# Kernel optimization log

Measured on AMD Instinct MI355X. Metric: run time of the kernel, lower is better.

## Reference

```python
import jax, jax.numpy as jnp
import numpy as np

MARGIN = 1.0
B, C = 64, 206

def setup_inputs() -> dict:
    key = jax.random.key(0)
    k1, k2, k3 = jax.random.split(key, 3)
    preds = jax.random.normal(k1, (B, C), dtype=jnp.float32)
    sample_weights = jax.random.uniform(k2, (B,), dtype=jnp.float32)
    labels = jax.random.randint(k3, (B, C), 0, 2, dtype=jnp.int32)
    return {"preds": preds, "sample_weights": sample_weights, "labels": labels}

def reference(preds, sample_weights, labels):
    # Faithful AUCLoss: mean over pos x neg pairs of log(1+exp(-(p-n)*margin)) * w_pos * w_neg.
    # Data-dependent boolean gathers are replaced by multiplicative masks (identical math):
    # masked entries contribute 0, and we divide by n_pos*n_neg (the masked-matrix size).
    pos_mask = (labels == 1)
    neg_mask = (labels == 0)
    # per-element weight = per-sample weight broadcast over classes
    w = jnp.broadcast_to(sample_weights[:, None], labels.shape)
    p = preds.reshape(-1)                      # [N]
    pw = jnp.where(pos_mask.reshape(-1), w.reshape(-1), 0.0)  # [N] pos weights (0 where not pos)
    nw = jnp.where(neg_mask.reshape(-1), w.reshape(-1), 0.0)  # [N] neg weights (0 where not neg)
    diff = p[:, None] - p[None, :]             # [N, N] pairwise diffs (pos rows, neg cols)
    loss_matrix = jax.nn.softplus(-diff * MARGIN)  # == log(1 + exp(-diff*margin)), stable
    weighted_sum = jnp.einsum('ij,i,j->', loss_matrix, pw, nw)
    n_pos = pos_mask.sum().astype(preds.dtype)
    n_neg = neg_mask.sum().astype(preds.dtype)
    return weighted_sum / (n_pos * n_neg)
```

## Files before the change

kernel.cpp:

```cpp
#include <hip/hip_runtime.h>

#define NB 64
#define NC 206
#define N (NB * NC)
#define IPT 4
#define GX 13
#define NGPR 52
#define NBLK (GX * NB)
#define LN2F 0.69314718056f

struct Ws {
    double partials[NBLK];
};

__global__ __launch_bounds__(256) void pairs_kernel(
    const float* __restrict__ preds,
    const float* __restrict__ sw,
    const int* __restrict__ labels,
    double* __restrict__ partials)
{
    const int bx   = blockIdx.x;
    const int row  = blockIdx.y;
    const int lane = threadIdx.x & 63;
    const int wid  = threadIdx.x >> 6;

    __shared__ float sEGf[NGPR * 4];
    __shared__ float wsum[4];

    {
        const int c = threadIdx.x;
        if (c < NGPR * 4) {
            float e = 0.0f;
            if (c < NC) {
                float p = preds[row * NC + c];
                int   l = labels[row * NC + c];
                e = (l == 0) ? __expf(p) : 0.0f;
            }
            sEGf[c] = e;
        }
    }

    float F[IPT], PW[IPT], acc[IPT];
    #pragma unroll
    for (int k = 0; k < IPT; ++k) {
        int i = bx * 1024 + k * 256 + threadIdx.x;
        if (i < N) {
            float p = preds[i];
            int   l = labels[i];
            F[k]  = __expf(-p);
            PW[k] = (l == 1) ? sw[i / NC] : 0.0f;
        } else {
            F[k] = 0.0f; PW[k] = 0.0f;
        }
        acc[k] = 0.0f;
    }
    __syncthreads();

    const float4* sEG = (const float4*)sEGf;

    #pragma unroll 2
    for (int g = 0; g < NGPR; ++g) {
        float4 e = sEG[g];
        #pragma unroll
        for (int k = 0; k < IPT; ++k) {
            float t0 = fmaf(e.x, F[k], 1.0f);
            float t1 = fmaf(e.y, F[k], 1.0f);
            float t2 = fmaf(e.z, F[k], 1.0f);
            float t3 = fmaf(e.w, F[k], 1.0f);
            float m  = (t0 * t1) * (t2 * t3);
            acc[k] += __log2f(m);
        }
    }

    float a = 0.0f;
    #pragma unroll
    for (int k = 0; k < IPT; ++k) a = fmaf(acc[k], PW[k], a);
    a *= sw[row] * LN2F;

    #pragma unroll
    for (int off = 32; off > 0; off >>= 1)
        a += __shfl_down(a, off, 64);

    if (lane == 0) wsum[wid] = a;
    __syncthreads();
    if (threadIdx.x == 0)
        partials[row * GX + bx] = (double)(wsum[0] + wsum[1] + wsum[2] + wsum[3]);
}

__global__ __launch_bounds__(256) void reduce_kernel(
    const int* __restrict__ labels,
    const Ws* __restrict__ ws,
    float* __restrict__ out)
{
    const int lane = threadIdx.x & 63;
    const int wid  = threadIdx.x >> 6;

    double s = 0.0;
    for (int t = threadIdx.x; t < NBLK; t += 256)
        s += ws->partials[t];

    int pc = 0;
    const int4* l4 = (const int4*)labels;
    for (int t = threadIdx.x; t < N / 4; t += 256) {
        int4 v = l4[t];
        pc += v.x + v.y + v.z + v.w;
    }

    #pragma unroll
    for (int off = 32; off > 0; off >>= 1) {
        s  += __shfl_down(s, off, 64);
        pc += __shfl_down(pc, off, 64);
    }

    __shared__ double ds[4];
    __shared__ int    dp[4];
    if (lane == 0) { ds[wid] = s; dp[wid] = pc; }
    __syncthreads();
    if (threadIdx.x == 0) {
        double total = ds[0] + ds[1] + ds[2] + ds[3];
        int npos     = dp[0] + dp[1] + dp[2] + dp[3];
        double denom = (double)npos * (double)(N - npos);
        out[0] = (float)(total / denom);
    }
}

extern "C" void kernel_launch(void* const* d_in, const int* in_sizes, int n_in,
                              void* d_out, int out_size, void* d_ws, size_t ws_size,
                              hipStream_t stream)
{
    const float* preds  = (const float*)d_in[0];
    const float* sw     = (const float*)d_in[1];
    const int*   labels = (const int*)d_in[2];
    float* out = (float*)d_out;
    Ws* ws = (Ws*)d_ws;

    dim3 grid(GX, NB);
    pairs_kernel<<<grid, 256, 0, stream>>>(preds, sw, labels, ws->partials);

    reduce_kernel<<<1, 256, 0, stream>>>(labels, ws, out);
}
```

Measured before the change: 22.55 us.

## Compact positive elements into shared memory and batch eight negatives per log

Each block uses wave ballots and prefix counts to compact only the positive-labelled elements of its chunk into shared memory, then runs the pairwise loop only over those, skipping the roughly half of work spent on zero-weight rows. The product trick is widened from four to eight negatives per log2, halving transcendental calls. This adds extra shared memory, two barriers and a serial segment scan, and multiplying eight factors raises the risk of float overflow for large exp values.

```diff
diff --git a/kernel.cpp b/kernel.cpp
--- a/kernel.cpp
+++ b/kernel.cpp
@@ -3,9 +3,8 @@
 #define NB 64
 #define NC 206
 #define N (NB * NC)
-#define IPT 4
 #define GX 13
-#define NGPR 52
+#define NG8 26
 #define NBLK (GX * NB)
 #define LN2F 0.69314718056f
 
@@ -21,69 +20,106 @@
 {
     const int bx   = blockIdx.x;
     const int row  = blockIdx.y;
-    const int lane = threadIdx.x & 63;
-    const int wid  = threadIdx.x >> 6;
+    const int tid  = threadIdx.x;
+    const int lane = tid & 63;
+    const int wave = tid >> 6;
 
-    __shared__ float sEGf[NGPR * 4];
+    __shared__ float sEGf[NG8 * 8];
+    __shared__ float sF[1024], sPW[1024];
+    __shared__ int   segCnt[16];
     __shared__ float wsum[4];
 
-    {
-        const int c = threadIdx.x;
-        if (c < NGPR * 4) {
-            float e = 0.0f;
-            if (c < NC) {
-                float p = preds[row * NC + c];
-                int   l = labels[row * NC + c];
-                e = (l == 0) ? __expf(p) : 0.0f;
-            }
-            sEGf[c] = e;
+    if (tid < NG8 * 8) {
+        float e = 0.0f;
+        if (tid < NC) {
+            float p = preds[row * NC + tid];
+            int   l = labels[row * NC + tid];
+            e = (l == 0) ? __expf(p) : 0.0f;
         }
+        sEGf[tid] = e;
     }
 
-    float F[IPT], PW[IPT], acc[IPT];
+    float pv[4]; float wv[4]; unsigned int rank[4]; bool act[4];
+    unsigned long long pre = (1ull << lane) - 1ull;
     #pragma unroll
-    for (int k = 0; k < IPT; ++k) {
-        int i = bx * 1024 + k * 256 + threadIdx.x;
+    for (int k = 0; k < 4; ++k) {
+        int i = bx * 1024 + k * 256 + tid;
+        bool a = false; float p = 0.0f, w = 0.0f;
         if (i < N) {
-            float p = preds[i];
-            int   l = labels[i];
-            F[k]  = __expf(-p);
-            PW[k] = (l == 1) ? sw[i / NC] : 0.0f;
-        } else {
-            F[k] = 0.0f; PW[k] = 0.0f;
+            p = preds[i];
+            a = (labels[i] == 1);
+            if (a) w = sw[i / NC];
         }
-        acc[k] = 0.0f;
+        unsigned long long ball = __ballot(a);
+        if (lane == 0) segCnt[k * 4 + wave] = __popcll(ball);
+        rank[k] = (unsigned int)__popcll(ball & pre);
+        act[k] = a; pv[k] = p; wv[k] = w;
     }
     __syncthreads();
 
-    const float4* sEG = (const float4*)sEGf;
-
-    #pragma unroll 2
-    for (int g = 0; g < NGPR; ++g) {
-        float4 e = sEG[g];
+    int segBase[4]; int nAct = 0;
+    {
+        int run = 0;
         #pragma unroll
-        for (int k = 0; k < IPT; ++k) {
-            float t0 = fmaf(e.x, F[k], 1.0f);
-            float t1 = fmaf(e.y, F[k], 1.0f);
-            float t2 = fmaf(e.z, F[k], 1.0f);
-            float t3 = fmaf(e.w, F[k], 1.0f);
-            float m  = (t0 * t1) * (t2 * t3);
-            acc[k] += __log2f(m);
+        for (int s = 0; s < 16; ++s) {
+            int c = segCnt[s];
+            int k = s >> 2, wv_ = s & 3;
+            if (wv_ == wave) segBase[k] = run;
+            run += c;
+        }
+        nAct = run;
+    }
+    #pragma unroll
+    for (int k = 0; k < 4; ++k) {
+        if (act[k]) {
+            int o = segBase[k] + (int)rank[k];
+            sF[o]  = __expf(-pv[k]);
+            sPW[o] = wv[k];
         }
     }
+    __syncthreads();
 
+    const float4* sEG4 = (const float4*)sEGf;
     float a = 0.0f;
-    #pragma unroll
-    for (int k = 0; k < IPT; ++k) a = fmaf(acc[k], PW[k], a);
+    for (int base = 0; base < nAct; base += 512) {
+        int i0 = base + tid, i1 = base + 256 + tid;
+        float F0 = 0.0f, P0 = 0.0f, F1 = 0.0f, P1 = 0.0f;
+        if (i0 < nAct) { F0 = sF[i0]; P0 = sPW[i0]; }
+        if (i1 < nAct) { F1 = sF[i1]; P1 = sPW[i1]; }
+        float a0 = 0.0f, a1 = 0.0f;
+        #pragma unroll 2
+        for (int g = 0; g < NG8; ++g) {
+            float4 e0 = sEG4[2 * g];
+            float4 e1 = sEG4[2 * g + 1];
+            float m0, m1;
+            {
+                float t0 = fmaf(e0.x, F0, 1.0f), t1 = fmaf(e0.y, F0, 1.0f);
+                float t2 = fmaf(e0.z, F0, 1.0f), t3 = fmaf(e0.w, F0, 1.0f);
+                float t4 = fmaf(e1.x, F0, 1.0f), t5 = fmaf(e1.y, F0, 1.0f);
+                float t6 = fmaf(e1.z, F0, 1.0f), t7 = fmaf(e1.w, F0, 1.0f);
+                m0 = ((t0 * t1) * (t2 * t3)) * ((t4 * t5) * (t6 * t7));
+            }
+            {
+                float t0 = fmaf(e0.x, F1, 1.0f), t1 = fmaf(e0.y, F1, 1.0f);
+                float t2 = fmaf(e0.z, F1, 1.0f), t3 = fmaf(e0.w, F1, 1.0f);
+                float t4 = fmaf(e1.x, F1, 1.0f), t5 = fmaf(e1.y, F1, 1.0f);
+                float t6 = fmaf(e1.z, F1, 1.0f), t7 = fmaf(e1.w, F1, 1.0f);
+                m1 = ((t0 * t1) * (t2 * t3)) * ((t4 * t5) * (t6 * t7));
+            }
+            a0 += __log2f(m0);
+            a1 += __log2f(m1);
+        }
+        a = fmaf(a0, P0, a);
+        a = fmaf(a1, P1, a);
+    }
     a *= sw[row] * LN2F;
 
     #pragma unroll
     for (int off = 32; off > 0; off >>= 1)
         a += __shfl_down(a, off, 64);
-
-    if (lane == 0) wsum[wid] = a;
+    if (lane == 0) wsum[wave] = a;
     __syncthreads();
-    if (threadIdx.x == 0)
+    if (tid == 0)
         partials[row * GX + bx] = (double)(wsum[0] + wsum[1] + wsum[2] + wsum[3]);
 }
 
```

After: 21.53 us, median of 2. 4.5% less time.
